# Optimization experiments

Hardware: AMD Instinct MI355X
Metric: run time of the kernel (lower is better)

The kernel has to match this reference:

```python
import jax, jax.numpy as jnp
import numpy as np
from jax import lax

H_SIZE = 2048
NUM_K = 16
NUM_V = 32
DK = 128
DV = 128
KDIM = NUM_K * DK      # 2048
VDIM = NUM_V * DV      # 4096
KCONV = 4
RMS_EPS = 1e-6
L2_EPS = 1e-6


def l2norm(x, eps=L2_EPS):
    # matches torch l2norm: x * rsqrt(sum(x^2, -1) + eps)
    return x * lax.rsqrt(jnp.sum(x * x, axis=-1, keepdims=True) + eps)


def setup_inputs() -> dict:
    key = jax.random.key(0)
    ks = jax.random.split(key, 7)
    B, S = 2, 1024
    conv_dim = 2 * KDIM + VDIM  # 8192
    return {
        "hidden_states": jax.random.normal(ks[0], (B, S, H_SIZE), jnp.float32),
        "w_qkvz": jax.random.normal(ks[1], (H_SIZE, 2 * KDIM + 2 * VDIM), jnp.float32) * 0.02,
        "w_ba": jax.random.normal(ks[2], (H_SIZE, 2 * NUM_V), jnp.float32) * 0.02,
        "conv_w": jax.random.normal(ks[3], (conv_dim, 1, KCONV), jnp.float32) * 0.2,  # depthwise [C,1,K]
        "dt_bias": jnp.ones((NUM_V,), jnp.float32),
        "A_log": jnp.log(jax.random.uniform(ks[4], (NUM_V,), jnp.float32, 0.5, 8.0)),
        "norm_w": jnp.ones((DV,), jnp.float32),
        "w_out": jax.random.normal(ks[5], (VDIM, H_SIZE), jnp.float32) * 0.02,
    }


def _forward(hidden_states, w_qkvz, w_ba, conv_w, dt_bias, A_log, norm_w, w_out):
    B, S, _ = hidden_states.shape
    rf = NUM_V // NUM_K  # GQA repeat factor = 2

    # input projections
    qkvz = hidden_states @ w_qkvz                                  # [B,S,12288]
    ba = hidden_states @ w_ba                                      # [B,S,64]

    # fix_query_key_value_ordering: group per k-head then split
    qkvz = qkvz.reshape(B, S, NUM_K, 2 * DK + 2 * rf * DV)
    q, k, v, z = jnp.split(qkvz, [DK, 2 * DK, 2 * DK + rf * DV], axis=3)
    ba = ba.reshape(B, S, NUM_K, 2 * rf)
    b, a = jnp.split(ba, [rf], axis=3)
    v = v.reshape(B, S, NUM_V, DV)
    z = z.reshape(B, S, NUM_V, DV)
    b = b.reshape(B, S, NUM_V)
    a = a.reshape(B, S, NUM_V)

    # depthwise causal conv over [q|k|v] channels + silu
    mixed = jnp.concatenate(
        [q.reshape(B, S, KDIM), k.reshape(B, S, KDIM), v.reshape(B, S, VDIM)], axis=-1
    )                                                              # [B,S,conv_dim]
    x = mixed.transpose(0, 2, 1)                                   # [B,C,S]
    x = jnp.pad(x, ((0, 0), (0, 0), (KCONV - 1, 0)))
    x = lax.conv_general_dilated(x, conv_w, window_strides=(1,), padding="VALID",
                                 feature_group_count=x.shape[1])
    x = jax.nn.silu(x).transpose(0, 2, 1)                          # [B,S,conv_dim]

    q, k, v = jnp.split(x, [KDIM, 2 * KDIM], axis=-1)
    q = q.reshape(B, S, NUM_K, DK)
    k = k.reshape(B, S, NUM_K, DK)
    v = v.reshape(B, S, NUM_V, DV)

    beta = jax.nn.sigmoid(b)                                       # [B,S,NUM_V]
    g = -jnp.exp(A_log) * jax.nn.softplus(a + dt_bias)             # log-decay [B,S,NUM_V]

    if rf > 1:
        q = jnp.repeat(q, rf, axis=2)                              # [B,S,NUM_V,DK]
        k = jnp.repeat(k, rf, axis=2)
    q = l2norm(q) * (DK ** -0.5)
    k = l2norm(k)

    # gated delta rule recurrence over time via lax.scan
    S0 = jnp.zeros((B, NUM_V, DK, DV), q.dtype)

    def step(state, inp):
        q_t, k_t, v_t, g_t, b_t = inp                              # [B,H,dk]/[B,H,dv]/[B,H]
        state = state * jnp.exp(g_t)[..., None, None]              # decay
        kv_mem = jnp.einsum("bhkv,bhk->bhv", state, k_t)
        delta = (v_t - kv_mem) * b_t[..., None]
        state = state + jnp.einsum("bhk,bhv->bhkv", k_t, delta)
        o = jnp.einsum("bhkv,bhk->bhv", state, q_t)
        return state, o

    xs = (jnp.moveaxis(q, 1, 0), jnp.moveaxis(k, 1, 0), jnp.moveaxis(v, 1, 0),
          jnp.moveaxis(g, 1, 0), jnp.moveaxis(beta, 1, 0))
    _, out = lax.scan(step, S0, xs)
    out = jnp.moveaxis(out, 0, 1)                                  # [B,S,NUM_V,DV]

    # gated RMSNorm (gate applied before normalization, Mamba2 style)
    xg = out * jax.nn.silu(z)
    y = xg * lax.rsqrt(jnp.mean(xg * xg, axis=-1, keepdims=True) + RMS_EPS) * norm_w
    y = y.reshape(B, S, VDIM)
    return y @ w_out                                               # [B,S,H_SIZE]


def reference(hidden_states, w_qkvz, w_ba, conv_w, dt_bias, A_log, norm_w, w_out):
    return _forward(hidden_states, w_qkvz, w_ba, conv_w, dt_bias, A_log, norm_w, w_out)
```

## Files before the change

### kernel.cpp

```cpp
#include <hip/hip_runtime.h>
#include <stdint.h>

#define AS1 __attribute__((address_space(1)))
#define AS3 __attribute__((address_space(3)))

typedef __bf16 bf16x8 __attribute__((ext_vector_type(8)));
typedef float f32x4 __attribute__((ext_vector_type(4)));

static __device__ __forceinline__ float bf2f(unsigned short u) {
    union { unsigned int i; float f; } x; x.i = ((unsigned int)u) << 16; return x.f;
}
static __device__ __forceinline__ unsigned short f2bf(float f) {
    union { float f; unsigned int i; } x; x.f = f;
    unsigned int u = x.i;
    unsigned int r = (u + 0x7fffu + ((u >> 16) & 1u)) >> 16;
    return (unsigned short)r;
}

static __device__ __forceinline__ void gll16(const void* g, void* l) {
    __builtin_amdgcn_global_load_lds((const AS1 unsigned int*)g,
                                     (AS3 unsigned int*)l, 16, 0, 0);
}

__global__ __launch_bounds__(256) void cvt_bf16_kernel(
    const float* __restrict__ src, unsigned short* __restrict__ dst, int n4) {
    int i = blockIdx.x * 256 + threadIdx.x;
    if (i >= n4) return;
    float4 v = ((const float4*)src)[i];
    ushort4 o;
    o.x = f2bf(v.x); o.y = f2bf(v.y); o.z = f2bf(v.z); o.w = f2bf(v.w);
    ((ushort4*)dst)[i] = o;
}

__global__ __launch_bounds__(256) void transpose_cvt_kernel(
    const float* __restrict__ src, unsigned short* __restrict__ dst, int R, int C) {
    __shared__ float tile[32][33];
    int x = threadIdx.x & 31, y = threadIdx.x >> 5;
    int c0 = blockIdx.x * 32, r0 = blockIdx.y * 32;
#pragma unroll
    for (int i = 0; i < 4; i++)
        tile[y + i * 8][x] = src[(size_t)(r0 + y + i * 8) * C + (c0 + x)];
    __syncthreads();
#pragma unroll
    for (int i = 0; i < 4; i++)
        dst[(size_t)(c0 + y + i * 8) * R + (r0 + x)] = f2bf(tile[x][y + i * 8]);
}

template <int STORE_BF16>
__global__ __launch_bounds__(256) void gemm_bt_kernel(
    const unsigned short* __restrict__ A, const unsigned short* __restrict__ Bt,
    void* __restrict__ C, int M, int N, int K) {
    __shared__ __align__(16) unsigned short As[128 * 32];
    __shared__ __align__(16) unsigned short Bs[128 * 32];
    int tid = threadIdx.x;
    int lane = tid & 63;
    int w = tid >> 6;
    int m0 = blockIdx.y * 128;
    int n0 = blockIdx.x * 128;
    int zz = blockIdx.z;
    int Kz = K / gridDim.z;
    int qd = lane >> 4, rc = lane & 15;
    int wm = (w >> 1) * 64, wn = (w & 1) * 64;

    f32x4 acc[4][4];
#pragma unroll
    for (int i = 0; i < 4; i++)
#pragma unroll
        for (int j = 0; j < 4; j++)
#pragma unroll
            for (int r = 0; r < 4; r++) acc[i][j][r] = 0.f;

    int s0 = w * 128 + lane;
    int s1 = s0 + 64;
    int rA0 = s0 >> 2, cs0 = (s0 & 3) * 8;
    int rA1 = s1 >> 2, cs1 = (s1 & 3) * 8;
    const unsigned short* a0 = A + (size_t)(m0 + rA0) * K + cs0 + (size_t)zz * Kz;
    const unsigned short* a1 = A + (size_t)(m0 + rA1) * K + cs1 + (size_t)zz * Kz;
    const unsigned short* b0 = Bt + (size_t)(n0 + rA0) * K + cs0 + (size_t)zz * Kz;
    const unsigned short* b1 = Bt + (size_t)(n0 + rA1) * K + cs1 + (size_t)zz * Kz;
    unsigned short* lA0 = As + s0 * 8;
    unsigned short* lA1 = As + s1 * 8;
    unsigned short* lB0 = Bs + s0 * 8;
    unsigned short* lB1 = Bs + s1 * 8;

    for (int k0 = 0; k0 < Kz; k0 += 32) {
        __syncthreads();
        gll16(a0 + k0, lA0);
        gll16(a1 + k0, lA1);
        gll16(b0 + k0, lB0);
        gll16(b1 + k0, lB1);
        __syncthreads();
        bf16x8 af[4], bfr[4];
#pragma unroll
        for (int i = 0; i < 4; i++)
            af[i] = *(const bf16x8*)(As + (wm + i * 16 + rc) * 32 + qd * 8);
#pragma unroll
        for (int i = 0; i < 4; i++)
            bfr[i] = *(const bf16x8*)(Bs + (wn + i * 16 + rc) * 32 + qd * 8);
#pragma unroll
        for (int i = 0; i < 4; i++)
#pragma unroll
            for (int j = 0; j < 4; j++)
                acc[i][j] = __builtin_amdgcn_mfma_f32_16x16x32_bf16(af[i], bfr[j], acc[i][j], 0, 0, 0);
    }

#pragma unroll
    for (int i = 0; i < 4; i++)
#pragma unroll
        for (int j = 0; j < 4; j++)
#pragma unroll
            for (int r = 0; r < 4; r++) {
                int row = m0 + wm + i * 16 + qd * 4 + r;
                int col = n0 + wn + j * 16 + rc;
                if (STORE_BF16)
                    ((unsigned short*)C)[(size_t)row * N + col] = f2bf(acc[i][j][r]);
                else
                    ((float*)C)[(size_t)zz * M * N + (size_t)row * N + col] = acc[i][j][r];
            }
}

__global__ __launch_bounds__(256) void add_out_kernel(
    const float* __restrict__ p, float* __restrict__ out, int n4) {
    int i = blockIdx.x * 256 + threadIdx.x;
    if (i >= n4) return;
    float4 a = ((const float4*)p)[i];
    float4 b = ((const float4*)(p + (size_t)n4 * 4))[i];
    ((float4*)out)[i] = make_float4(a.x + b.x, a.y + b.y, a.z + b.z, a.w + b.w);
}

__global__ __launch_bounds__(256) void bag_kernel(
    const float* __restrict__ hs, const float* __restrict__ w_ba,
    const float* __restrict__ A_log, const float* __restrict__ dt_bias,
    float* __restrict__ gg, float* __restrict__ bb) {
    int w = threadIdx.x >> 6, lane = threadIdx.x & 63;
    int r0 = blockIdx.x * 8 + w * 2;
    const float* h0 = hs + (size_t)r0 * 2048;
    float a0 = 0.f, a1 = 0.f;
    for (int k = 0; k < 2048; k++) {
        float wv = w_ba[k * 64 + lane];
        a0 += h0[k] * wv;
        a1 += h0[2048 + k] * wv;
    }
    int h = lane >> 2, idx = lane & 3;
    int vh = h * 2 + (idx & 1);
    float accs[2] = {a0, a1};
#pragma unroll
    for (int j = 0; j < 2; j++) {
        int t = r0 + j;
        float acc = accs[j];
        if (idx < 2) {
            bb[t * 32 + vh] = 1.f / (1.f + expf(-acc));
        } else {
            float x = acc + dt_bias[vh];
            float sp = fmaxf(x, 0.f) + log1pf(expf(-fabsf(x)));
            gg[t * 32 + vh] = -expf(A_log[vh]) * sp;
        }
    }
}

__global__ __launch_bounds__(256) void conv_kernel(
    const unsigned short* __restrict__ qkvz, const float* __restrict__ conv_w,
    unsigned short* __restrict__ qb, unsigned short* __restrict__ kb,
    float* __restrict__ vv) {
    __shared__ float xs[8192];
    __shared__ float rs[32];
    int t = blockIdx.x;
    int s = t & 1023;
    int tid = threadIdx.x;
    size_t rowbase = (size_t)t * 12288;
#pragma unroll
    for (int i = 0; i < 4; i++) {
        int c = (i * 256 + tid) * 8;
        int d = c & 127;
        int col;
        if (c < 2048) col = (c >> 7) * 768 + d;
        else if (c < 4096) col = ((c - 2048) >> 7) * 768 + 128 + d;
        else { int vh2 = (c - 4096) >> 7; col = (vh2 >> 1) * 768 + 256 + (vh2 & 1) * 128 + d; }
        float wts[8][4];
#pragma unroll
        for (int e = 0; e < 8; e++) {
            float4 t4 = *(const float4*)(conv_w + (size_t)(c + e) * 4);
            wts[e][0] = t4.x; wts[e][1] = t4.y; wts[e][2] = t4.z; wts[e][3] = t4.w;
        }
        float acc[8] = {0.f, 0.f, 0.f, 0.f, 0.f, 0.f, 0.f, 0.f};
#pragma unroll
        for (int j = 0; j < 4; j++) {
            int ss = s - 3 + j;
            if (ss >= 0) {
                uint4 u = *(const uint4*)(qkvz + rowbase + (size_t)(j - 3) * 12288 + col);
                const unsigned short* us = (const unsigned short*)&u;
#pragma unroll
                for (int e = 0; e < 8; e++) acc[e] += bf2f(us[e]) * wts[e][j];
            }
        }
#pragma unroll
        for (int e = 0; e < 8; e++) xs[c + e] = acc[e] / (1.f + expf(-acc[e]));
    }
    __syncthreads();
    {
        int seg = tid >> 3, part = tid & 7;
        const float* pp = xs + seg * 128 + part * 16;
        float s2 = 0.f;
#pragma unroll
        for (int j = 0; j < 16; j++) s2 += pp[j] * pp[j];
        s2 += __shfl_xor(s2, 1);
        s2 += __shfl_xor(s2, 2);
        s2 += __shfl_xor(s2, 4);
        if (part == 0) rs[seg] = rsqrtf(s2 + 1e-6f);
    }
    __syncthreads();
    const float QS = 0.08838834764831845f;
#pragma unroll
    for (int i = 0; i < 4; i++) {
        int c = (i * 256 + tid) * 8;
        float x[8];
#pragma unroll
        for (int e = 0; e < 8; e++) x[e] = xs[c + e];
        if (c < 4096) {
            float sc = (c < 2048) ? rs[c >> 7] * QS : rs[((c - 2048) >> 7) + 16];
            uint4 o;
            o.x = (unsigned)f2bf(x[0] * sc) | ((unsigned)f2bf(x[1] * sc) << 16);
            o.y = (unsigned)f2bf(x[2] * sc) | ((unsigned)f2bf(x[3] * sc) << 16);
            o.z = (unsigned)f2bf(x[4] * sc) | ((unsigned)f2bf(x[5] * sc) << 16);
            o.w = (unsigned)f2bf(x[6] * sc) | ((unsigned)f2bf(x[7] * sc) << 16);
            if (c < 2048) *(uint4*)(qb + (size_t)t * 2048 + c) = o;
            else *(uint4*)(kb + (size_t)t * 2048 + c - 2048) = o;
        } else {
            float* vp = vv + (size_t)t * 4096 + c - 4096;
            *(float4*)vp = make_float4(x[0], x[1], x[2], x[3]);
            *(float4*)(vp + 4) = make_float4(x[4], x[5], x[6], x[7]);
        }
    }
}

__global__ __launch_bounds__(256, 2) void prep_kernel(
    const unsigned short* __restrict__ qb, const unsigned short* __restrict__ kb,
    const float* __restrict__ vv, const float* __restrict__ gg,
    const float* __restrict__ bb,
    unsigned short* __restrict__ Wg, unsigned short* __restrict__ DlT,
    unsigned short* __restrict__ KtT, unsigned short* __restrict__ Pt,
    float* __restrict__ lamg, float* __restrict__ l64g) {
    __shared__ __align__(16) unsigned short Tb[64 * 72];
    __shared__ __align__(16) unsigned short Xw[4][64 * 72];
    __shared__ float Td[4 * 16 * 17];
    __shared__ float RHSw[4][16 * 68];
    __shared__ float cc[64], bet[64], lam_s[64], ex64[64];

    int bid = blockIdx.x;
    int ch = bid & 15, bh = bid >> 4;
    int vh = bh & 31, b = bh >> 5;
    int hk = vh >> 1;
    int t0 = b * 1024 + ch * 64;
    int tid = threadIdx.x, wv = tid >> 6, lane = tid & 63;
    int qd = lane >> 4, rc = lane & 15;
    int rowb = (wv & 1) * 32;
    size_t obase = (size_t)bid * 8192;
    size_t pbase = (size_t)bid * 4096;

    if (tid < 64) {
        float x = gg[(size_t)(t0 + tid) * 32 + vh];
#pragma unroll
        for (int ofs = 1; ofs < 64; ofs <<= 1) {
            float up = __shfl_up(x, ofs, 64);
            if (tid >= ofs) x += up;
        }
        cc[tid] = x;
        float l = __expf(x);
        lam_s[tid] = l;
        float tot = __shfl(x, 63, 64);
        ex64[tid] = __expf(tot - x);
        bet[tid] = bb[(size_t)(t0 + tid) * 32 + vh];
        lamg[(size_t)bid * 64 + tid] = l;
        if (tid == 0) l64g[bid] = __expf(tot);
    }
    __syncthreads();

    {
        const unsigned short* src = (wv >= 2) ? qb : kb;
        f32x4 acc[2][4];
#pragma unroll
        for (int tm = 0; tm < 2; tm++)
#pragma unroll
            for (int tn = 0; tn < 4; tn++)
#pragma unroll
                for (int r = 0; r < 4; r++) acc[tm][tn][r] = 0.f;
#pragma unroll
        for (int ks = 0; ks < 4; ks++) {
            bf16x8 af[2], bfr[4];
#pragma unroll
            for (int tm = 0; tm < 2; tm++) {
                int row = rowb + tm * 16 + rc;
                af[tm] = *(const bf16x8*)(src + ((size_t)(t0 + row) * 16 + hk) * 128 + ks * 32 + qd * 8);
            }
#pragma unroll
            for (int tn = 0; tn < 4; tn++)
                bfr[tn] = *(const bf16x8*)(kb + ((size_t)(t0 + tn * 16 + rc) * 16 + hk) * 128 + ks * 32 + qd * 8);
#pragma unroll
            for (int tm = 0; tm < 2; tm++)
#pragma unroll
                for (int tn = 0; tn < 4; tn++)
                    acc[tm][tn] = __builtin_amdgcn_mfma_f32_16x16x32_bf16(af[tm], bfr[tn], acc[tm][tn], 0, 0, 0);
        }
        if (wv < 2) {
#pragma unroll
            for (int tm = 0; tm < 2; tm++)
#pragma unroll
                for (int tn = 0; tn < 4; tn++)
#pragma unroll
                    for (int r = 0; r < 4; r++) {
                        int i = rowb + tm * 16 + qd * 4 + r;
                        int j = tn * 16 + rc;
                        float val = acc[tm][tn][r];
                        float tv = 0.f;
                        if (i > j) tv = bet[i] * __expf(cc[i] - cc[j]) * val;
                        Tb[i * 72 + j] = f2bf(-tv);
                        if ((i >> 4) == (j >> 4) && i > j)
                            Td[(i >> 4) * 272 + (i & 15) * 17 + (j & 15)] = tv;
                    }
        } else {
#pragma unroll
            for (int tm = 0; tm < 2; tm++)
#pragma unroll
                for (int tn = 0; tn < 4; tn++)
#pragma unroll
                    for (int r = 0; r < 4; r++) {
                        int i = rowb + tm * 16 + qd * 4 + r;
                        int j = tn * 16 + rc;
                        float ev = (i >= j) ? __expf(cc[i] - cc[j]) : 0.f;
                        Pt[pbase + i * 64 + j] = f2bf(ev * acc[tm][tn][r]);
                    }
        }
    }
    {
        int dk = tid >> 1, half = tid & 1;
#pragma unroll
        for (int j = 0; j < 4; j++) {
            unsigned short tmp[8];
#pragma unroll
            for (int e = 0; e < 8; e++) {
                int tok = half * 32 + j * 8 + e;
                tmp[e] = f2bf(bf2f(kb[((size_t)(t0 + tok) * 16 + hk) * 128 + dk]) * ex64[tok]);
            }
            *(uint4*)(KtT + obase + dk * 64 + half * 32 + j * 8) = *(const uint4*)tmp;
        }
    }
    __syncthreads();

    {
        int cb = wv;
        unsigned short* Xb = Xw[wv];
        float* RHS = RHSw[wv];
        for (int z = lane; z < 64 * 72 / 2; z += 64) ((unsigned int*)Xb)[z] = 0u;
#pragma unroll
        for (int B = 0; B < 4; B++) {
            f32x4 tacc[4];
#pragma unroll
            for (int cf = 0; cf < 4; cf++)
#pragma unroll
                for (int r = 0; r < 4; r++) {
                    int i = B * 16 + qd * 4 + r;
                    int c = cf * 16 + rc;
                    float v;
                    if (cb < 2)
                        v = bet[i] * vv[((size_t)(t0 + i) * 32 + vh) * 128 + cb * 64 + c];
                    else
                        v = bet[i] * lam_s[i] * bf2f(kb[((size_t)(t0 + i) * 16 + hk) * 128 + (cb - 2) * 64 + c]);
                    tacc[cf][r] = v;
                }
            __builtin_amdgcn_s_waitcnt(0xc07f);
            const int nks = (B + 1) >> 1;
#pragma unroll
            for (int ks = 0; ks < 2; ks++) {
                if (ks >= nks) break;
                bf16x8 af = *(const bf16x8*)&Tb[(B * 16 + rc) * 72 + ks * 32 + qd * 8];
#pragma unroll
                for (int cf = 0; cf < 4; cf++) {
                    bf16x8 bf_ = *(const bf16x8*)&Xb[(cf * 16 + rc) * 72 + ks * 32 + qd * 8];
                    tacc[cf] = __builtin_amdgcn_mfma_f32_16x16x32_bf16(af, bf_, tacc[cf], 0, 0, 0);
                }
            }
#pragma unroll
            for (int cf = 0; cf < 4; cf++)
#pragma unroll
                for (int r = 0; r < 4; r++)
                    RHS[(qd * 4 + r) * 68 + cf * 16 + rc] = tacc[cf][r];
            __builtin_amdgcn_s_waitcnt(0xc07f);
            {
                float d[16];
#pragma unroll
                for (int i2 = 0; i2 < 16; i2++) d[i2] = RHS[i2 * 68 + lane];
#pragma unroll
                for (int i2 = 1; i2 < 16; i2++)
#pragma unroll
                    for (int j2 = 0; j2 < i2; j2++)
                        d[i2] -= Td[B * 272 + i2 * 17 + j2] * d[j2];
#pragma unroll
                for (int i2 = 0; i2 < 16; i2++)
                    Xb[lane * 72 + B * 16 + i2] = f2bf(d[i2]);
            }
        }
        __builtin_amdgcn_s_waitcnt(0xc07f);
        if (cb < 2) {
#pragma unroll
            for (int j = 0; j < 8; j++) {
                uint4 u = *(const uint4*)&Xb[lane * 72 + j * 8];
                *(uint4*)(DlT + obase + (size_t)(cb * 64 + lane) * 64 + j * 8) = u;
            }
        } else {
#pragma unroll
            for (int dq = 0; dq < 8; dq++) {
                unsigned short tmp[8];
#pragma unroll
                for (int e = 0; e < 8; e++)
                    tmp[e] = Xb[(dq * 8 + e) * 72 + lane];
                *(uint4*)(Wg + obase + (size_t)lane * 128 + (cb - 2) * 64 + dq * 8) = *(const uint4*)tmp;
            }
        }
    }
}

__global__ __launch_bounds__(256, 2) void recb_kernel(
    const unsigned short* __restrict__ qb, const float* __restrict__ lamg,
    const float* __restrict__ l64g, const unsigned short* __restrict__ Wg,
    const unsigned short* __restrict__ DlT, const unsigned short* __restrict__ KtT,
    const unsigned short* __restrict__ Pt, float* __restrict__ oo) {
    __shared__ __align__(16) unsigned short St[16 * 136];
    __shared__ __align__(16) unsigned short Dls[16 * 72];
    int bid = blockIdx.x;
    int slice = bid >> 6;
    int rest = bid & 63;
    int vh = rest & 31, b = rest >> 5;
    int bh = b * 32 + vh;
    int hk = vh >> 1, dvo = slice * 16, tb = b * 1024;
    int tid = threadIdx.x, wv = tid >> 6, lane = tid & 63;
    int qd = lane >> 4, rc = lane & 15;

    f32x4 sacc[2];
#pragma unroll
    for (int tm = 0; tm < 2; tm++)
#pragma unroll
        for (int r = 0; r < 4; r++) sacc[tm][r] = 0.f;
    for (int z = tid; z < 16 * 136 / 2; z += 256) ((unsigned int*)St)[z] = 0u;
    __syncthreads();

#pragma unroll 1
    for (int ch = 0; ch < 16; ch++) {
        int bhch = bh * 16 + ch;
        size_t obase = (size_t)bhch * 8192;
        size_t pbase = (size_t)bhch * 4096;
        int t0 = tb + ch * 64;
        if (tid < 128) {
            int row = tid >> 3, t8 = (tid & 7) * 8;
            uint4 u = *(const uint4*)(DlT + obase + (dvo + row) * 64 + t8);
            *(uint4*)&Dls[row * 72 + t8] = u;
        }
        __syncthreads();
        {
            f32x4 uacc;
#pragma unroll
            for (int r = 0; r < 4; r++) uacc[r] = 0.f;
#pragma unroll
            for (int ks = 0; ks < 4; ks++) {
                bf16x8 a_ = *(const bf16x8*)&St[rc * 136 + ks * 32 + qd * 8];
                bf16x8 b_ = *(const bf16x8*)(Wg + obase + (size_t)(wv * 16 + rc) * 128 + ks * 32 + qd * 8);
                uacc = __builtin_amdgcn_mfma_f32_16x16x32_bf16(a_, b_, uacc, 0, 0, 0);
            }
#pragma unroll
            for (int r = 0; r < 4; r++) {
                int idx = (qd * 4 + r) * 72 + wv * 16 + rc;
                Dls[idx] = f2bf(bf2f(Dls[idx]) - uacc[r]);
            }
        }
        __syncthreads();
        {
            f32x4 qacc;
#pragma unroll
            for (int r = 0; r < 4; r++) qacc[r] = 0.f;
#pragma unroll
            for (int ks = 0; ks < 4; ks++) {
                bf16x8 a_ = *(const bf16x8*)(qb + ((size_t)(t0 + wv * 16 + rc) * 16 + hk) * 128 + ks * 32 + qd * 8);
                bf16x8 b_ = *(const bf16x8*)&St[rc * 136 + ks * 32 + qd * 8];
                qacc = __builtin_amdgcn_mfma_f32_16x16x32_bf16(a_, b_, qacc, 0, 0, 0);
            }
            bf16x8 bd[2];
#pragma unroll
            for (int ks = 0; ks < 2; ks++)
                bd[ks] = *(const bf16x8*)&Dls[rc * 72 + ks * 32 + qd * 8];
            f32x4 oacc;
#pragma unroll
            for (int r = 0; r < 4; r++)
                oacc[r] = lamg[(size_t)bhch * 64 + wv * 16 + qd * 4 + r] * qacc[r];
#pragma unroll
            for (int ks = 0; ks < 2; ks++) {
                bf16x8 a_ = *(const bf16x8*)(Pt + pbase + (size_t)(wv * 16 + rc) * 64 + ks * 32 + qd * 8);
                oacc = __builtin_amdgcn_mfma_f32_16x16x32_bf16(a_, bd[ks], oacc, 0, 0, 0);
            }
#pragma unroll
            for (int r = 0; r < 4; r++)
                oo[((size_t)(t0 + wv * 16 + qd * 4 + r) * 32 + vh) * 128 + dvo + rc] = oacc[r];
            float l64 = l64g[bhch];
#pragma unroll
            for (int tm = 0; tm < 2; tm++) {
#pragma unroll
                for (int r = 0; r < 4; r++) sacc[tm][r] *= l64;
#pragma unroll
                for (int ks = 0; ks < 2; ks++) {
                    bf16x8 a_ = *(const bf16x8*)(KtT + obase + (size_t)(wv * 32 + tm * 16 + rc) * 64 + ks * 32 + qd * 8);
                    sacc[tm] = __builtin_amdgcn_mfma_f32_16x16x32_bf16(a_, bd[ks], sacc[tm], 0, 0, 0);
                }
            }
        }
        __syncthreads();
#pragma unroll
        for (int tm = 0; tm < 2; tm++)
#pragma unroll
            for (int r = 0; r < 4; r++)
                St[rc * 136 + wv * 32 + tm * 16 + qd * 4 + r] = f2bf(sacc[tm][r]);
        __syncthreads();
    }
}

__global__ __launch_bounds__(256) void norm_kernel(
    const float* __restrict__ oo, const unsigned short* __restrict__ qkvz,
    const float* __restrict__ norm_w, unsigned short* __restrict__ yb) {
    int w = threadIdx.x >> 6, lane = threadIdx.x & 63;
    int g = blockIdx.x * 4 + w;
    int t = g >> 5, vh = g & 31;
    size_t ob = (size_t)g * 128;
    size_t zb = (size_t)t * 12288 + (size_t)(vh >> 1) * 768 + 512 + (vh & 1) * 128;
    float x0 = oo[ob + lane], x1 = oo[ob + 64 + lane];
    float z0 = bf2f(qkvz[zb + lane]), z1 = bf2f(qkvz[zb + 64 + lane]);
    float xg0 = x0 * (z0 / (1.f + expf(-z0)));
    float xg1 = x1 * (z1 / (1.f + expf(-z1)));
    float s = xg0 * xg0 + xg1 * xg1;
    s += __shfl_xor(s, 1);
    s += __shfl_xor(s, 2);
    s += __shfl_xor(s, 4);
    s += __shfl_xor(s, 8);
    s += __shfl_xor(s, 16);
    s += __shfl_xor(s, 32);
    float r = rsqrtf(s * (1.f / 128.f) + 1e-6f);
    size_t y0 = (size_t)t * 4096 + (size_t)vh * 128;
    yb[y0 + lane] = f2bf(xg0 * r * norm_w[lane]);
    yb[y0 + 64 + lane] = f2bf(xg1 * r * norm_w[64 + lane]);
}

extern "C" void kernel_launch(void* const* d_in, const int* in_sizes, int n_in,
                              void* d_out, int out_size, void* d_ws, size_t ws_size,
                              hipStream_t stream) {
    const float* hs      = (const float*)d_in[0];
    const float* w_qkvz  = (const float*)d_in[1];
    const float* w_ba    = (const float*)d_in[2];
    const float* conv_w  = (const float*)d_in[3];
    const float* dt_bias = (const float*)d_in[4];
    const float* A_log   = (const float*)d_in[5];
    const float* norm_w  = (const float*)d_in[6];
    const float* w_out   = (const float*)d_in[7];
    float* out = (float*)d_out;
    (void)in_sizes; (void)n_in; (void)out_size; (void)ws_size;

    char* p = (char*)d_ws;
    auto alloc = [&](size_t b) { char* r = p; p += (b + 255) & ~(size_t)255; return r; };
    float* gg = (float*)alloc(2048ull * 32 * 4);
    float* bb = (float*)alloc(2048ull * 32 * 4);
    unsigned short* hsb  = (unsigned short*)alloc(2048ull * 2048 * 2);
    unsigned short* wqT  = (unsigned short*)alloc(12288ull * 2048 * 2);
    unsigned short* woT  = (unsigned short*)alloc(2048ull * 4096 * 2);
    unsigned short* qkvz = (unsigned short*)alloc(2048ull * 12288 * 2);
    unsigned short* qb16 = (unsigned short*)alloc(2048ull * 2048 * 2);
    unsigned short* kb16 = (unsigned short*)alloc(2048ull * 2048 * 2);
    float* vv = (float*)alloc(2048ull * 4096 * 4);
    float* oo = (float*)alloc(2048ull * 4096 * 4);
    unsigned short* yb = (unsigned short*)alloc(2048ull * 4096 * 2);
    unsigned short* Wg  = (unsigned short*)alloc(1024ull * 8192 * 2);
    unsigned short* DlT = (unsigned short*)alloc(1024ull * 8192 * 2);
    unsigned short* KtT = (unsigned short*)alloc(1024ull * 8192 * 2);
    unsigned short* Pt  = (unsigned short*)alloc(1024ull * 4096 * 2);
    float* lamg = (float*)alloc(1024ull * 64 * 4);
    float* l64g = (float*)alloc(1024ull * 4);
    float* gpart = (float*)wqT;

    cvt_bf16_kernel<<<4096, 256, 0, stream>>>(hs, hsb, 2048 * 2048 / 4);
    transpose_cvt_kernel<<<dim3(12288 / 32, 2048 / 32), 256, 0, stream>>>(w_qkvz, wqT, 2048, 12288);
    transpose_cvt_kernel<<<dim3(2048 / 32, 4096 / 32), 256, 0, stream>>>(w_out, woT, 4096, 2048);
    gemm_bt_kernel<1><<<dim3(96, 16, 1), 256, 0, stream>>>(hsb, wqT, qkvz, 2048, 12288, 2048);
    bag_kernel<<<256, 256, 0, stream>>>(hs, w_ba, A_log, dt_bias, gg, bb);
    conv_kernel<<<2048, 256, 0, stream>>>(qkvz, conv_w, qb16, kb16, vv);
    prep_kernel<<<1024, 256, 0, stream>>>(qb16, kb16, vv, gg, bb, Wg, DlT, KtT, Pt, lamg, l64g);
    recb_kernel<<<512, 256, 0, stream>>>(qb16, lamg, l64g, Wg, DlT, KtT, Pt, oo);
    norm_kernel<<<16384, 256, 0, stream>>>(oo, qkvz, norm_w, yb);
    gemm_bt_kernel<0><<<dim3(16, 16, 2), 256, 0, stream>>>(yb, woT, gpart, 2048, 2048, 4096);
    add_out_kernel<<<4096, 256, 0, stream>>>(gpart, out, 2048 * 2048 / 4);
}
```

Baseline: 759.9 us.

## Replace 128x128 GEMM with pipelined 256x256 double-buffered MFMA kernel

Both bf16 GEMMs now use a new 512-thread kernel. It computes a 256x256 output tile per block and stages 64-wide K slices into a 128KB swizzled LDS double buffer through global_load_lds. Loads for upcoming tiles are interleaved with four quadrant MFMA phases, using explicit vmcnt waits, barriers and setprio. The input projection maps blocks to XCDs for L2 locality, and the output projection uses split-K of 4 with a four-way reduction kernel. The workspace is reordered so the larger fp32 partial buffer can overflow into dead buffers without overwriting woT. The cost is heavy register and LDS use, fragile hand-written synchronization, and more partial-sum traffic for the output GEMM.

```diff
diff --git a/kernel.cpp b/kernel.cpp
--- a/kernel.cpp
+++ b/kernel.cpp
@@ -46,86 +46,186 @@
         dst[(size_t)(c0 + y + i * 8) * R + (r0 + x)] = f2bf(tile[x][y + i * 8]);
 }
 
-template <int STORE_BF16>
-__global__ __launch_bounds__(256) void gemm_bt_kernel(
+template <int MODE>
+__global__ __launch_bounds__(512, 2) void gemm256_kernel(
     const unsigned short* __restrict__ A, const unsigned short* __restrict__ Bt,
-    void* __restrict__ C, int M, int N, int K) {
-    __shared__ __align__(16) unsigned short As[128 * 32];
-    __shared__ __align__(16) unsigned short Bs[128 * 32];
+    void* __restrict__ C, int M, int N, int K, int Ksl) {
+    __shared__ __align__(16) unsigned short SH[65536];
     int tid = threadIdx.x;
-    int lane = tid & 63;
-    int w = tid >> 6;
-    int m0 = blockIdx.y * 128;
-    int n0 = blockIdx.x * 128;
-    int zz = blockIdx.z;
-    int Kz = K / gridDim.z;
+    int lane = tid & 63, w = tid >> 6;
+    int wr = w >> 2, wc = w & 3;
     int qd = lane >> 4, rc = lane & 15;
-    int wm = (w >> 1) * 64, wn = (w & 1) * 64;
-
-    f32x4 acc[4][4];
-#pragma unroll
-    for (int i = 0; i < 4; i++)
+
+    int m0, n0, zz = 0;
+    if (MODE == 0) {
+        int wg = blockIdx.x;
+        int xcd = wg & 7, loc = wg >> 3;
+        m0 = (loc / 6) * 256;
+        n0 = (xcd * 6 + loc % 6) * 256;
+    } else {
+        int wg = blockIdx.x;
+        zz = wg >> 6;
+        int loc = wg & 63;
+        m0 = (loc >> 3) * 256;
+        n0 = (loc & 7) * 256;
+    }
+    const int NT = Ksl >> 6;
+    const int sK = K << 7;
+
+    size_t sr[2];
+#pragma unroll
+    for (int j = 0; j < 2; j++) {
+        int bu = j * 4096 + tid * 8;
+        int sub = bu >> 9;
+        int b = bu & 511;
+        int bp = b ^ (((b >> 8) & 1) << 4);
+        int row = ((sub >> 1) << 4) + (bp >> 5);
+        int col = ((sub & 1) << 5) + (bp & 31);
+        sr[j] = (size_t)row * K + col;
+    }
+    const unsigned short* Ab = A + (size_t)m0 * K + (size_t)zz * Ksl;
+    const unsigned short* Bb = Bt + (size_t)n0 * K + (size_t)zz * Ksl;
+
+    const int foff = (rc * 32 + qd * 8) ^ (((rc >> 3) & 1) << 4);
+    const int Ah = wr;
+    const int Bh = wc >> 1;
+    const int brow4 = (wc & 1) * 4;
+
+    f32x4 acc[8][4];
+#pragma unroll
+    for (int i = 0; i < 8; i++)
 #pragma unroll
         for (int j = 0; j < 4; j++)
 #pragma unroll
             for (int r = 0; r < 4; r++) acc[i][j][r] = 0.f;
 
-    int s0 = w * 128 + lane;
-    int s1 = s0 + 64;
-    int rA0 = s0 >> 2, cs0 = (s0 & 3) * 8;
-    int rA1 = s1 >> 2, cs1 = (s1 & 3) * 8;
-    const unsigned short* a0 = A + (size_t)(m0 + rA0) * K + cs0 + (size_t)zz * Kz;
-    const unsigned short* a1 = A + (size_t)(m0 + rA1) * K + cs1 + (size_t)zz * Kz;
-    const unsigned short* b0 = Bt + (size_t)(n0 + rA0) * K + cs0 + (size_t)zz * Kz;
-    const unsigned short* b1 = Bt + (size_t)(n0 + rA1) * K + cs1 + (size_t)zz * Kz;
-    unsigned short* lA0 = As + s0 * 8;
-    unsigned short* lA1 = As + s1 * 8;
-    unsigned short* lB0 = Bs + s0 * 8;
-    unsigned short* lB1 = Bs + s1 * 8;
-
-    for (int k0 = 0; k0 < Kz; k0 += 32) {
-        __syncthreads();
-        gll16(a0 + k0, lA0);
-        gll16(a1 + k0, lA1);
-        gll16(b0 + k0, lB0);
-        gll16(b1 + k0, lB1);
-        __syncthreads();
-        bf16x8 af[4], bfr[4];
-#pragma unroll
-        for (int i = 0; i < 4; i++)
-            af[i] = *(const bf16x8*)(As + (wm + i * 16 + rc) * 32 + qd * 8);
-#pragma unroll
-        for (int i = 0; i < 4; i++)
-            bfr[i] = *(const bf16x8*)(Bs + (wn + i * 16 + rc) * 32 + qd * 8);
-#pragma unroll
-        for (int i = 0; i < 4; i++)
-#pragma unroll
-            for (int j = 0; j < 4; j++)
-                acc[i][j] = __builtin_amdgcn_mfma_f32_16x16x32_bf16(af[i], bfr[j], acc[i][j], 0, 0, 0);
-    }
-
-#pragma unroll
-    for (int i = 0; i < 4; i++)
-#pragma unroll
-        for (int j = 0; j < 4; j++)
-#pragma unroll
-            for (int r = 0; r < 4; r++) {
-                int row = m0 + wm + i * 16 + qd * 4 + r;
-                int col = n0 + wn + j * 16 + rc;
-                if (STORE_BF16)
-                    ((unsigned short*)C)[(size_t)row * N + col] = f2bf(acc[i][j][r]);
-                else
-                    ((float*)C)[(size_t)zz * M * N + (size_t)row * N + col] = acc[i][j][r];
-            }
-}
-
-__global__ __launch_bounds__(256) void add_out_kernel(
+    bf16x8 aq[4][2], bq[4][2];
+
+#define STG(mat, h, t)                                                        \
+    {                                                                         \
+        const unsigned short* s_ = ((mat) ? Bb : Ab) + (h) * sK + (t) * 64;   \
+        int d_ = ((mat) << 15) + (((((t) & 1) * 2 + (h))) << 13) + tid * 8;   \
+        gll16(s_ + sr[0], &SH[d_]);                                           \
+        gll16(s_ + sr[1], &SH[d_ + 4096]);                                    \
+    }
+
+#define LDAQ(p, QR)                                                           \
+    {                                                                         \
+        int ab_ = ((p) * 2 + Ah) * 8192 + (QR) * 4096 + foff;                 \
+        _Pragma("unroll") for (int fi = 0; fi < 4; fi++)                      \
+            _Pragma("unroll") for (int ks = 0; ks < 2; ks++)                  \
+                aq[fi][ks] = *(const bf16x8*)&SH[ab_ + (fi * 2 + ks) * 512];  \
+    }
+
+#define LDBQ(p)                                                               \
+    {                                                                         \
+        int bb_ = 32768 + ((p) * 2 + Bh) * 8192 + brow4 * 1024 + foff;        \
+        _Pragma("unroll") for (int fg = 0; fg < 4; fg++)                      \
+            _Pragma("unroll") for (int ks = 0; ks < 2; ks++)                  \
+                bq[fg][ks] = *(const bf16x8*)&SH[bb_ + (fg * 2 + ks) * 512];  \
+    }
+
+#define MFMAQ(QR, QC)                                                         \
+    {                                                                         \
+        _Pragma("unroll") for (int fi = 0; fi < 4; fi++)                      \
+            _Pragma("unroll") for (int fj = 0; fj < 2; fj++)                  \
+                _Pragma("unroll") for (int ks = 0; ks < 2; ks++)              \
+                    acc[(QR) * 4 + fi][(QC) * 2 + fj] =                       \
+                        __builtin_amdgcn_mfma_f32_16x16x32_bf16(              \
+                            aq[fi][ks], bq[(QC) * 2 + fj][ks],                \
+                            acc[(QR) * 4 + fi][(QC) * 2 + fj], 0, 0, 0);      \
+    }
+
+#define FENCE asm volatile("" ::: "memory")
+#define BARRIER { FENCE; __builtin_amdgcn_s_barrier(); FENCE; }
+#define LGKM0 asm volatile("s_waitcnt lgkmcnt(0)" ::: "memory")
+
+    STG(0, 0, 0); STG(0, 1, 0); STG(1, 0, 0); STG(1, 1, 0);
+    STG(1, 0, 1); STG(1, 1, 1); STG(0, 0, 1);
+    asm volatile("s_waitcnt vmcnt(6)" ::: "memory");
+    BARRIER;
+
+    for (int g = 0; g < NT; ++g) {
+        const int p = g & 1;
+        LDAQ(p, 0);
+        LDBQ(p);
+        if (g + 1 < NT) STG(0, 1, g + 1);
+        BARRIER; LGKM0;
+        __builtin_amdgcn_s_setprio(1);
+        MFMAQ(0, 0);
+        __builtin_amdgcn_s_setprio(0);
+        BARRIER;
+        if (g + 2 < NT) STG(1, 0, g + 2);
+        BARRIER; LGKM0;
+        __builtin_amdgcn_s_setprio(1);
+        MFMAQ(0, 1);
+        __builtin_amdgcn_s_setprio(0);
+        BARRIER;
+        LDAQ(p, 1);
+        if (g + 2 < NT) STG(1, 1, g + 2);
+        BARRIER; LGKM0;
+        __builtin_amdgcn_s_setprio(1);
+        MFMAQ(1, 0);
+        __builtin_amdgcn_s_setprio(0);
+        BARRIER;
+        if (g + 2 < NT) STG(0, 0, g + 2);
+        if (g < NT - 2) { asm volatile("s_waitcnt vmcnt(6)" ::: "memory"); }
+        else            { asm volatile("s_waitcnt vmcnt(0)" ::: "memory"); }
+        BARRIER; LGKM0;
+        __builtin_amdgcn_s_setprio(1);
+        MFMAQ(1, 1);
+        __builtin_amdgcn_s_setprio(0);
+        BARRIER;
+    }
+
+#undef STG
+#undef LDAQ
+#undef LDBQ
+#undef MFMAQ
+#undef FENCE
+#undef BARRIER
+#undef LGKM0
+
+    if (MODE == 0) {
+        unsigned short* Cp = (unsigned short*)C;
+#pragma unroll
+        for (int mi = 0; mi < 8; mi++) {
+            int row = m0 + wr * 128 + mi * 16 + qd * 4;
+#pragma unroll
+            for (int fg = 0; fg < 4; fg++) {
+                int col = n0 + wc * 64 + fg * 16 + rc;
+#pragma unroll
+                for (int r = 0; r < 4; r++)
+                    Cp[(size_t)(row + r) * N + col] = f2bf(acc[mi][fg][r]);
+            }
+        }
+    } else {
+        float* Cf = (float*)C + (size_t)zz * M * N;
+#pragma unroll
+        for (int mi = 0; mi < 8; mi++) {
+            int row = m0 + wr * 128 + mi * 16 + qd * 4;
+#pragma unroll
+            for (int fg = 0; fg < 4; fg++) {
+                int col = n0 + wc * 64 + fg * 16 + rc;
+#pragma unroll
+                for (int r = 0; r < 4; r++)
+                    Cf[(size_t)(row + r) * N + col] = acc[mi][fg][r];
+            }
+        }
+    }
+}
+
+__global__ __launch_bounds__(256) void add_out4_kernel(
     const float* __restrict__ p, float* __restrict__ out, int n4) {
     int i = blockIdx.x * 256 + threadIdx.x;
     if (i >= n4) return;
+    size_t st = (size_t)n4 * 4;
     float4 a = ((const float4*)p)[i];
-    float4 b = ((const float4*)(p + (size_t)n4 * 4))[i];
-    ((float4*)out)[i] = make_float4(a.x + b.x, a.y + b.y, a.z + b.z, a.w + b.w);
+    float4 b = ((const float4*)(p + st))[i];
+    float4 c = ((const float4*)(p + 2 * st))[i];
+    float4 d = ((const float4*)(p + 3 * st))[i];
+    ((float4*)out)[i] = make_float4(a.x + b.x + c.x + d.x, a.y + b.y + c.y + d.y,
+                                    a.z + b.z + c.z + d.z, a.w + b.w + c.w + d.w);
 }
 
 __global__ __launch_bounds__(256) void bag_kernel(
@@ -564,8 +664,8 @@
     float* gg = (float*)alloc(2048ull * 32 * 4);
     float* bb = (float*)alloc(2048ull * 32 * 4);
     unsigned short* hsb  = (unsigned short*)alloc(2048ull * 2048 * 2);
+    unsigned short* woT  = (unsigned short*)alloc(2048ull * 4096 * 2);
     unsigned short* wqT  = (unsigned short*)alloc(12288ull * 2048 * 2);
-    unsigned short* woT  = (unsigned short*)alloc(2048ull * 4096 * 2);
     unsigned short* qkvz = (unsigned short*)alloc(2048ull * 12288 * 2);
     unsigned short* qb16 = (unsigned short*)alloc(2048ull * 2048 * 2);
     unsigned short* kb16 = (unsigned short*)alloc(2048ull * 2048 * 2);
@@ -583,12 +683,12 @@
     cvt_bf16_kernel<<<4096, 256, 0, stream>>>(hs, hsb, 2048 * 2048 / 4);
     transpose_cvt_kernel<<<dim3(12288 / 32, 2048 / 32), 256, 0, stream>>>(w_qkvz, wqT, 2048, 12288);
     transpose_cvt_kernel<<<dim3(2048 / 32, 4096 / 32), 256, 0, stream>>>(w_out, woT, 4096, 2048);
-    gemm_bt_kernel<1><<<dim3(96, 16, 1), 256, 0, stream>>>(hsb, wqT, qkvz, 2048, 12288, 2048);
+    gemm256_kernel<0><<<384, 512, 0, stream>>>(hsb, wqT, qkvz, 2048, 12288, 2048, 2048);
     bag_kernel<<<256, 256, 0, stream>>>(hs, w_ba, A_log, dt_bias, gg, bb);
     conv_kernel<<<2048, 256, 0, stream>>>(qkvz, conv_w, qb16, kb16, vv);
     prep_kernel<<<1024, 256, 0, stream>>>(qb16, kb16, vv, gg, bb, Wg, DlT, KtT, Pt, lamg, l64g);
     recb_kernel<<<512, 256, 0, stream>>>(qb16, lamg, l64g, Wg, DlT, KtT, Pt, oo);
     norm_kernel<<<16384, 256, 0, stream>>>(oo, qkvz, norm_w, yb);
-    gemm_bt_kernel<0><<<dim3(16, 16, 2), 256, 0, stream>>>(yb, woT, gpart, 2048, 2048, 4096);
-    add_out_kernel<<<4096, 256, 0, stream>>>(gpart, out, 2048 * 2048 / 4);
-}
+    gemm256_kernel<1><<<256, 512, 0, stream>>>(yb, woT, gpart, 2048, 2048, 4096, 1024);
+    add_out4_kernel<<<4096, 256, 0, stream>>>(gpart, out, 2048 * 2048 / 4);
+}
```

After: 733.5 us. -3.5%, faster.
